# Kernel tuning notes

Measured on AMD Instinct MI355X. Metric: run time of the kernel, lower is better.

## Reference

```python
import jax, jax.numpy as jnp
import numpy as np

DIM = 256
HEADS = 8
DIM_HEAD = 32
INNER = HEADS * DIM_HEAD  # 256
EPS = 1e-5


def layer_norm(x, g, b):
    mu = jnp.mean(x, axis=-1, keepdims=True)
    var = jnp.var(x, axis=-1, keepdims=True)
    return (x - mu) * jax.lax.rsqrt(var + EPS) * g + b


def setup_inputs() -> dict:
    key = jax.random.key(0)
    ks = jax.random.split(key, 8)
    b, l, gx, gy, w1, w2 = 2, 5, 6, 8, 8, 8
    B, N = b * gx * gy, l * w1 * w2  # 96, 320
    x = jax.random.normal(ks[0], (b, l, gx, gy, w1, w2, DIM), dtype=jnp.float32)
    # context is the additive attention bias: [B, N, heads*N] -> (B,h,N,N)
    context = jax.random.normal(ks[1], (B, N, HEADS * N), dtype=jnp.float32) * 0.1
    s = 1.0 / np.sqrt(DIM)
    w_q = jax.random.normal(ks[2], (DIM, INNER), dtype=jnp.float32) * s
    w_kv = jax.random.normal(ks[3], (DIM, 2 * INNER), dtype=jnp.float32) * s
    w_out = jax.random.normal(ks[4], (INNER, DIM_HEAD), dtype=jnp.float32) * (1.0 / np.sqrt(INNER))
    ln_g = jnp.ones((DIM,), dtype=jnp.float32)
    ln_b = jnp.zeros((DIM,), dtype=jnp.float32)
    return {"x": x, "context": context, "w_q": w_q, "w_kv": w_kv,
            "w_out": w_out, "ln_g": ln_g, "ln_b": ln_b}


def reference(x, context, w_q, w_kv, w_out, ln_g, ln_b):
    b, l, gx, gy, w1, w2, d = x.shape
    # 'b l x y w1 w2 d -> (b x y) (l w1 w2) d'
    xs = jnp.transpose(x, (0, 2, 3, 1, 4, 5, 6)).reshape(b * gx * gy, l * w1 * w2, d)
    B, N, D = xs.shape
    xs = layer_norm(xs, ln_g, ln_b)
    q = (xs @ w_q).reshape(B, N, HEADS, DIM_HEAD).transpose(0, 2, 1, 3)   # b h n d
    kv = xs @ w_kv
    k, v = jnp.split(kv, 2, axis=-1)
    k = k.reshape(B, N, HEADS, DIM_HEAD).transpose(0, 2, 1, 3)
    v = v.reshape(B, N, HEADS, DIM_HEAD).transpose(0, 2, 1, 3)
    # bias mode with context: dots = q k^T (unscaled, faithful to source) + bias
    dots = jnp.einsum('bhnd,bhmd->bhnm', q, k)
    bias = context.reshape(B, N, HEADS, N).transpose(0, 2, 1, 3)          # b h n m
    dots = dots + bias
    attn = jax.nn.softmax(dots, axis=-1)
    out = jnp.einsum('bhnm,bhmd->bhnd', attn, v)                          # b h n d
    # 'b h (l w1 w2) d -> b l w1 w2 (h d)'
    out = out.transpose(0, 2, 1, 3).reshape(B, l, w1, w2, INNER)
    out = out @ w_out                                                     # -> dim_head
    # '(b x y) l w1 w2 d -> b l x y w1 w2 d'
    out = out.reshape(b, gx, gy, l, w1, w2, DIM_HEAD).transpose(0, 3, 1, 2, 4, 5, 6)
    return out
```

## Files before the change

### kernel.cpp

```cpp
#include <hip/hip_runtime.h>
#include <hip/hip_bf16.h>

#define BWIN 96
#define NTOK 320
#define DIMX 256
#define HEADS 8
#define DH 32
#define INNER 256
#define CTXW 2560
#define MPAD 328
#define ROWS_T 30720

typedef __bf16 bf16x8 __attribute__((ext_vector_type(8)));
typedef __bf16 bf16x4 __attribute__((ext_vector_type(4)));
typedef float f32x4 __attribute__((ext_vector_type(4)));

__global__ __launch_bounds__(256) void k_pre(
    const float* __restrict__ wq, const float* __restrict__ wkv,
    const float* __restrict__ x, const float* __restrict__ g,
    const float* __restrict__ bt, __bf16* __restrict__ wT,
    __bf16* __restrict__ y)
{
    const int t = threadIdx.x;
    if (blockIdx.x < 768) {
        const int col = blockIdx.x;
        float v;
        if (col < 256)      v = wq[t * 256 + col];
        else if (col < 512) v = wkv[t * 512 + (col - 256)];
        else                v = wkv[t * 512 + 256 + (col - 512)];
        wT[(size_t)col * 256 + t] = (__bf16)v;
        return;
    }
    const int wave = t >> 6, lane = t & 63;
    const int row = (blockIdx.x - 768) * 4 + wave;
    const int bb = row / NTOK, n = row % NTOK;
    const int b_idx = bb / 48, x_idx = (bb % 48) >> 3, y_idx = bb & 7;
    const int l_idx = n >> 6, w1_idx = (n >> 3) & 7, w2_idx = n & 7;
    const size_t src =
        ((((((size_t)b_idx * 5 + l_idx) * 6 + x_idx) * 8 + y_idx) * 8 + w1_idx) * 8 + w2_idx) * (size_t)DIMX;

    const float4 xv = *(const float4*)(x + src + lane * 4);
    float s = xv.x + xv.y + xv.z + xv.w;
    float ss = xv.x * xv.x + xv.y * xv.y + xv.z * xv.z + xv.w * xv.w;
    #pragma unroll
    for (int o = 32; o > 0; o >>= 1) {
        s += __shfl_xor(s, o);
        ss += __shfl_xor(ss, o);
    }
    const float mu = s * (1.0f / DIMX);
    const float var = ss * (1.0f / DIMX) - mu * mu;
    const float rsig = rsqrtf(var + 1e-5f);
    const float4 g4 = *(const float4*)(g + lane * 4);
    const float4 b4 = *(const float4*)(bt + lane * 4);
    bf16x4 yo;
    yo[0] = (__bf16)((xv.x - mu) * rsig * g4.x + b4.x);
    yo[1] = (__bf16)((xv.y - mu) * rsig * g4.y + b4.y);
    yo[2] = (__bf16)((xv.z - mu) * rsig * g4.z + b4.z);
    yo[3] = (__bf16)((xv.w - mu) * rsig * g4.w + b4.w);
    *(bf16x4*)(y + (size_t)row * DIMX + lane * 4) = yo;
}

__global__ __launch_bounds__(256) void k_qkv(
    const __bf16* __restrict__ y, const __bf16* __restrict__ wT,
    __bf16* __restrict__ qhb, __bf16* __restrict__ khb, __bf16* __restrict__ vhb)
{
    __shared__ __bf16 yls[128][40];
    __shared__ __bf16 wls[128][40];
    const int t = threadIdx.x, wave = t >> 6, lane = t & 63;
    const int lr = lane & 15, lg = lane >> 4;
    const int wm = wave & 1, wn = wave >> 1;
    const int rbase = blockIdx.x * 128;
    const int cbase = blockIdx.y * 128;

    f32x4 acc[4][4];
    #pragma unroll
    for (int im = 0; im < 4; ++im)
        #pragma unroll
        for (int jn = 0; jn < 4; ++jn) acc[im][jn] = (f32x4){0.f, 0.f, 0.f, 0.f};

    const int srow = t >> 1, sseg = (t & 1) * 16;
    #pragma unroll
    for (int ks = 0; ks < 8; ++ks) {
        __syncthreads();
        #pragma unroll
        for (int j = 0; j < 2; ++j) {
            *(bf16x8*)&yls[srow][sseg + j * 8] =
                *(const bf16x8*)(y + (size_t)(rbase + srow) * DIMX + ks * 32 + sseg + j * 8);
            *(bf16x8*)&wls[srow][sseg + j * 8] =
                *(const bf16x8*)(wT + (size_t)(cbase + srow) * DIMX + ks * 32 + sseg + j * 8);
        }
        __syncthreads();

        bf16x8 yfr[4], wfr[4];
        #pragma unroll
        for (int jn = 0; jn < 4; ++jn) yfr[jn] = *(const bf16x8*)&yls[wm * 64 + jn * 16 + lr][lg * 8];
        #pragma unroll
        for (int im = 0; im < 4; ++im) wfr[im] = *(const bf16x8*)&wls[wn * 64 + im * 16 + lr][lg * 8];
        #pragma unroll
        for (int im = 0; im < 4; ++im)
            #pragma unroll
            for (int jn = 0; jn < 4; ++jn)
                acc[im][jn] = __builtin_amdgcn_mfma_f32_16x16x32_bf16(wfr[im], yfr[jn], acc[im][jn], 0, 0, 0);
    }

    #pragma unroll
    for (int im = 0; im < 4; ++im) {
        const int g = cbase + wn * 64 + im * 16 + lg * 4;
        const int which = g >> 8;
        __bf16* buf = (which == 0) ? qhb : (which == 1) ? khb : vhb;
        const int hh = (g & 255) >> 5, d = g & 31;
        #pragma unroll
        for (int jn = 0; jn < 4; ++jn) {
            const int row = rbase + wm * 64 + jn * 16 + lr;
            const int bb2 = row / NTOK, n2 = row % NTOK;
            bf16x4 p;
            #pragma unroll
            for (int i = 0; i < 4; ++i) p[i] = (__bf16)acc[im][jn][i];
            *(bf16x4*)(buf + ((size_t)(bb2 * 8 + hh) * NTOK + n2) * DH + d) = p;
        }
    }
}

__global__ __launch_bounds__(256) void k_vw(
    const __bf16* __restrict__ vhb, const float* __restrict__ wout,
    __bf16* __restrict__ vwt)
{
    const int t = threadIdx.x, wave = t >> 6, lane = t & 63;
    const int lr = lane & 15, lg = lane >> 4;
    const int bb = blockIdx.x, h = blockIdx.y;
    const int m0 = wave * 80;

    bf16x8 afr[2];
    #pragma unroll
    for (int rt = 0; rt < 2; ++rt)
        #pragma unroll
        for (int j = 0; j < 8; ++j)
            afr[rt][j] = (__bf16)wout[(h * 32 + lg * 8 + j) * 32 + rt * 16 + lr];

    const __bf16* vbase = vhb + (size_t)(bb * 8 + h) * NTOK * DH + lg * 8;
    __bf16* obase = vwt + ((size_t)(bb * HEADS + h) * DH) * NTOK;

    #pragma unroll
    for (int mt = 0; mt < 5; ++mt) {
        const int m = m0 + mt * 16 + lr;
        const bf16x8 bfr = *(const bf16x8*)(vbase + (size_t)m * DH);
        #pragma unroll
        for (int rt = 0; rt < 2; ++rt) {
            const f32x4 d4 = __builtin_amdgcn_mfma_f32_16x16x32_bf16(
                afr[rt], bfr, (f32x4){0.f, 0.f, 0.f, 0.f}, 0, 0, 0);
            #pragma unroll
            for (int i = 0; i < 4; ++i) {
                const int drow = rt * 16 + lg * 4 + i;
                obase[(size_t)drow * NTOK + m0 + mt * 16 + lr] = (__bf16)d4[i];
            }
        }
    }
}

__global__ __launch_bounds__(128) void k_attn(
    const __bf16* __restrict__ qhb, const __bf16* __restrict__ khb,
    const __bf16* __restrict__ vwt, const float* __restrict__ ctx,
    float* __restrict__ part)
{
    __shared__ __bf16 kls[NTOK][DH];
    __shared__ __bf16 vwls[DH][MPAD];
    __shared__ __bf16 ctxls[2][16][MPAD];
    const int t = threadIdx.x, wave = t >> 6, lane = t & 63;
    const int lr = lane & 15, lg = lane >> 4;
    const int h = blockIdx.x & 7, bb = blockIdx.x >> 3;
    const size_t panel = (size_t)(bb * 8 + h);

    const __bf16* kpan = khb + panel * NTOK * DH;
    #pragma unroll
    for (int i = 0; i < 10; ++i) {
        const int idx = i * 128 + t;
        *(bf16x8*)&kls[idx >> 2][(idx & 3) * 8] = *(const bf16x8*)(kpan + idx * 8);
    }
    const __bf16* vpan = vwt + panel * DH * NTOK;
    #pragma unroll
    for (int i = 0; i < 10; ++i) {
        const int idx = i * 128 + t;
        const int r = idx / 40, c = (idx % 40) * 8;
        *(bf16x8*)&vwls[r][c] = *(const bf16x8*)(vpan + r * NTOK + c);
    }
    __syncthreads();

    const float* cpan = ctx + (size_t)bb * NTOK * CTXW + h * NTOK;
    const __bf16* qpan = qhb + panel * NTOK * DH;
    float* ppan = part + ((size_t)h * ROWS_T + (size_t)bb * NTOK) * DH;

    float4 creg[20];
    {
        const float* cb = cpan + (size_t)(wave * 16) * CTXW;
        #pragma unroll
        for (int j = 0; j < 20; ++j) {
            const int f = j * 64 + lane, r = f / 80, c = f % 80;
            creg[j] = *(const float4*)(cb + (size_t)r * CTXW + c * 4);
        }
    }

    for (int it = 0; it < 10; ++it) {
        const int nw = (it * 2 + wave) * 16;

        #pragma unroll
        for (int j = 0; j < 20; ++j) {
            const int f = j * 64 + lane, r = f / 80, c = f % 80;
            bf16x4 b;
            b[0] = (__bf16)creg[j].x; b[1] = (__bf16)creg[j].y;
            b[2] = (__bf16)creg[j].z; b[3] = (__bf16)creg[j].w;
            *(bf16x4*)&ctxls[wave][r][c * 4] = b;
        }
        if (it < 9) {
            const float* cb = cpan + (size_t)((it * 2 + 2 + wave) * 16) * CTXW;
            #pragma unroll
            for (int j = 0; j < 20; ++j) {
                const int f = j * 64 + lane, r = f / 80, c = f % 80;
                creg[j] = *(const float4*)(cb + (size_t)r * CTXW + c * 4);
            }
        }

        const bf16x8 qfrag = *(const bf16x8*)(qpan + (size_t)(nw + lr) * DH + lg * 8);

        f32x4 s[20];
        #pragma unroll
        for (int mt = 0; mt < 20; ++mt) {
            const bf16x8 kfrag = *(const bf16x8*)&kls[mt * 16 + lr][lg * 8];
            s[mt] = __builtin_amdgcn_mfma_f32_16x16x32_bf16(kfrag, qfrag,
                                                            (f32x4){0.f, 0.f, 0.f, 0.f}, 0, 0, 0);
        }

        #pragma unroll
        for (int mt = 0; mt < 20; ++mt) {
            const bf16x4 c4 = *(const bf16x4*)&ctxls[wave][lr][mt * 16 + lg * 4];
            #pragma unroll
            for (int i = 0; i < 4; ++i) s[mt][i] += (float)c4[i];
        }

        float mx = -3e38f;
        #pragma unroll
        for (int mt = 0; mt < 20; ++mt)
            #pragma unroll
            for (int i = 0; i < 4; ++i) mx = fmaxf(mx, s[mt][i]);
        mx = fmaxf(mx, __shfl_xor(mx, 16));
        mx = fmaxf(mx, __shfl_xor(mx, 32));

        float sum = 0.f;
        #pragma unroll
        for (int mt = 0; mt < 20; ++mt) {
            bf16x4 p4;
            #pragma unroll
            for (int i = 0; i < 4; ++i) {
                const float e = __expf(s[mt][i] - mx);
                sum += e;
                p4[i] = (__bf16)e;
            }
            *(bf16x4*)&ctxls[wave][lr][mt * 16 + lg * 4] = p4;
        }
        sum += __shfl_xor(sum, 16);
        sum += __shfl_xor(sum, 32);
        const float rinv = 1.0f / sum;

        f32x4 o0 = {0.f, 0.f, 0.f, 0.f}, o1 = {0.f, 0.f, 0.f, 0.f};
        #pragma unroll
        for (int ks = 0; ks < 10; ++ks) {
            const bf16x8 pfrag = *(const bf16x8*)&ctxls[wave][lr][ks * 32 + lg * 8];
            const bf16x8 vf0 = *(const bf16x8*)&vwls[lr][ks * 32 + lg * 8];
            const bf16x8 vf1 = *(const bf16x8*)&vwls[16 + lr][ks * 32 + lg * 8];
            o0 = __builtin_amdgcn_mfma_f32_16x16x32_bf16(vf0, pfrag, o0, 0, 0, 0);
            o1 = __builtin_amdgcn_mfma_f32_16x16x32_bf16(vf1, pfrag, o1, 0, 0, 0);
        }

        float* pdst = ppan + (size_t)(nw + lr) * DH + lg * 4;
        f32x4 r0, r1;
        #pragma unroll
        for (int i = 0; i < 4; ++i) { r0[i] = o0[i] * rinv; r1[i] = o1[i] * rinv; }
        *(f32x4*)(pdst)      = r0;
        *(f32x4*)(pdst + 16) = r1;
    }
}

__global__ __launch_bounds__(256) void k_red(
    const float* __restrict__ part, float* __restrict__ out)
{
    const int idx = blockIdx.x * 256 + threadIdx.x;
    const int row = idx >> 3, q4 = (idx & 7) * 4;
    f32x4 a = {0.f, 0.f, 0.f, 0.f};
    #pragma unroll
    for (int h = 0; h < HEADS; ++h) {
        const f32x4 p = *(const f32x4*)(part + ((size_t)h * ROWS_T + row) * DH + q4);
        #pragma unroll
        for (int i = 0; i < 4; ++i) a[i] += p[i];
    }
    const int bb = row / NTOK, n = row % NTOK;
    const int b_idx = bb / 48, x_idx = (bb % 48) >> 3, y_idx = bb & 7;
    const int l_idx = n >> 6, w1_idx = (n >> 3) & 7, w2_idx = n & 7;
    const size_t dst =
        ((((((size_t)b_idx * 5 + l_idx) * 6 + x_idx) * 8 + y_idx) * 8 + w1_idx) * 8 + w2_idx) * (size_t)DH;
    *(f32x4*)(out + dst + q4) = a;
}

extern "C" void kernel_launch(void* const* d_in, const int* in_sizes, int n_in,
                              void* d_out, int out_size, void* d_ws, size_t ws_size,
                              hipStream_t stream) {
    const float* x    = (const float*)d_in[0];
    const float* ctx  = (const float*)d_in[1];
    const float* wq   = (const float*)d_in[2];
    const float* wkv  = (const float*)d_in[3];
    const float* wout = (const float*)d_in[4];
    const float* ln_g = (const float*)d_in[5];
    const float* ln_b = (const float*)d_in[6];
    float* out = (float*)d_out;

    const size_t SEG = (size_t)BWIN * NTOK * INNER;
    __bf16* qhb = (__bf16*)d_ws;
    __bf16* khb = qhb + SEG;
    __bf16* vhb = khb + SEG;
    __bf16* yb  = vhb + SEG;
    __bf16* wT  = yb + SEG;
    __bf16* vwt = wT + 768 * 256;
    float*  part = (float*)(vwt + SEG);

    const int ROWS = BWIN * NTOK;
    k_pre<<<768 + ROWS / 4, 256, 0, stream>>>(wq, wkv, x, ln_g, ln_b, wT, yb);
    k_qkv<<<dim3(ROWS / 128, 6), 256, 0, stream>>>(yb, wT, qhb, khb, vhb);
    k_vw<<<dim3(BWIN, HEADS), 256, 0, stream>>>(vhb, wout, vwt);
    k_attn<<<BWIN * HEADS, 128, 0, stream>>>(qhb, khb, vwt, ctx, part);
    k_red<<<ROWS * 8 / 256, 256, 0, stream>>>(part, out);
}
```

Measured before the change: 162.8 us.

## Fuse V·Wout projection into attention kernel and read K fragments from global

Removes the separate k_vw launch: each attention block now computes its V·Wout panel directly into shared memory with MFMA, avoiding the vwt workspace round trip. The K panel is no longer staged in LDS; kfrag loads come straight from global memory (likely cached in L1/L2). This saves one kernel launch and a global write/read of the projected V and frees LDS, possibly improving occupancy. The cost is redundant global K loads in every iteration and extra MFMA work at the start of each attention block.

```diff
diff --git a/kernel.cpp b/kernel.cpp
--- a/kernel.cpp
+++ b/kernel.cpp
@@ -121,48 +121,11 @@
     }
 }
 
-__global__ __launch_bounds__(256) void k_vw(
-    const __bf16* __restrict__ vhb, const float* __restrict__ wout,
-    __bf16* __restrict__ vwt)
-{
-    const int t = threadIdx.x, wave = t >> 6, lane = t & 63;
-    const int lr = lane & 15, lg = lane >> 4;
-    const int bb = blockIdx.x, h = blockIdx.y;
-    const int m0 = wave * 80;
-
-    bf16x8 afr[2];
-    #pragma unroll
-    for (int rt = 0; rt < 2; ++rt)
-        #pragma unroll
-        for (int j = 0; j < 8; ++j)
-            afr[rt][j] = (__bf16)wout[(h * 32 + lg * 8 + j) * 32 + rt * 16 + lr];
-
-    const __bf16* vbase = vhb + (size_t)(bb * 8 + h) * NTOK * DH + lg * 8;
-    __bf16* obase = vwt + ((size_t)(bb * HEADS + h) * DH) * NTOK;
-
-    #pragma unroll
-    for (int mt = 0; mt < 5; ++mt) {
-        const int m = m0 + mt * 16 + lr;
-        const bf16x8 bfr = *(const bf16x8*)(vbase + (size_t)m * DH);
-        #pragma unroll
-        for (int rt = 0; rt < 2; ++rt) {
-            const f32x4 d4 = __builtin_amdgcn_mfma_f32_16x16x32_bf16(
-                afr[rt], bfr, (f32x4){0.f, 0.f, 0.f, 0.f}, 0, 0, 0);
-            #pragma unroll
-            for (int i = 0; i < 4; ++i) {
-                const int drow = rt * 16 + lg * 4 + i;
-                obase[(size_t)drow * NTOK + m0 + mt * 16 + lr] = (__bf16)d4[i];
-            }
-        }
-    }
-}
-
 __global__ __launch_bounds__(128) void k_attn(
     const __bf16* __restrict__ qhb, const __bf16* __restrict__ khb,
-    const __bf16* __restrict__ vwt, const float* __restrict__ ctx,
-    float* __restrict__ part)
+    const __bf16* __restrict__ vhb, const float* __restrict__ wout,
+    const float* __restrict__ ctx, float* __restrict__ part)
 {
-    __shared__ __bf16 kls[NTOK][DH];
     __shared__ __bf16 vwls[DH][MPAD];
     __shared__ __bf16 ctxls[2][16][MPAD];
     const int t = threadIdx.x, wave = t >> 6, lane = t & 63;
@@ -170,23 +133,33 @@
     const int h = blockIdx.x & 7, bb = blockIdx.x >> 3;
     const size_t panel = (size_t)(bb * 8 + h);
 
-    const __bf16* kpan = khb + panel * NTOK * DH;
-    #pragma unroll
-    for (int i = 0; i < 10; ++i) {
-        const int idx = i * 128 + t;
-        *(bf16x8*)&kls[idx >> 2][(idx & 3) * 8] = *(const bf16x8*)(kpan + idx * 8);
-    }
-    const __bf16* vpan = vwt + panel * DH * NTOK;
-    #pragma unroll
-    for (int i = 0; i < 10; ++i) {
-        const int idx = i * 128 + t;
-        const int r = idx / 40, c = (idx % 40) * 8;
-        *(bf16x8*)&vwls[r][c] = *(const bf16x8*)(vpan + r * NTOK + c);
+    {
+        bf16x8 afr[2];
+        #pragma unroll
+        for (int rt = 0; rt < 2; ++rt)
+            #pragma unroll
+            for (int j = 0; j < 8; ++j)
+                afr[rt][j] = (__bf16)wout[(h * 32 + lg * 8 + j) * 32 + rt * 16 + lr];
+        const __bf16* vbase = vhb + panel * NTOK * DH + lg * 8;
+        #pragma unroll
+        for (int mt = 0; mt < 10; ++mt) {
+            const int m = wave * 160 + mt * 16 + lr;
+            const bf16x8 bfr = *(const bf16x8*)(vbase + (size_t)m * DH);
+            #pragma unroll
+            for (int rt = 0; rt < 2; ++rt) {
+                const f32x4 d4 = __builtin_amdgcn_mfma_f32_16x16x32_bf16(
+                    afr[rt], bfr, (f32x4){0.f, 0.f, 0.f, 0.f}, 0, 0, 0);
+                #pragma unroll
+                for (int i = 0; i < 4; ++i)
+                    vwls[rt * 16 + lg * 4 + i][wave * 160 + mt * 16 + lr] = (__bf16)d4[i];
+            }
+        }
     }
     __syncthreads();
 
     const float* cpan = ctx + (size_t)bb * NTOK * CTXW + h * NTOK;
     const __bf16* qpan = qhb + panel * NTOK * DH;
+    const __bf16* kpan = khb + panel * NTOK * DH;
     float* ppan = part + ((size_t)h * ROWS_T + (size_t)bb * NTOK) * DH;
 
     float4 creg[20];
@@ -224,7 +197,7 @@
         f32x4 s[20];
         #pragma unroll
         for (int mt = 0; mt < 20; ++mt) {
-            const bf16x8 kfrag = *(const bf16x8*)&kls[mt * 16 + lr][lg * 8];
+            const bf16x8 kfrag = *(const bf16x8*)(kpan + (size_t)(mt * 16 + lr) * DH + lg * 8);
             s[mt] = __builtin_amdgcn_mfma_f32_16x16x32_bf16(kfrag, qfrag,
                                                             (f32x4){0.f, 0.f, 0.f, 0.f}, 0, 0, 0);
         }
@@ -317,13 +290,11 @@
     __bf16* vhb = khb + SEG;
     __bf16* yb  = vhb + SEG;
     __bf16* wT  = yb + SEG;
-    __bf16* vwt = wT + 768 * 256;
-    float*  part = (float*)(vwt + SEG);
+    float*  part = (float*)(wT + 768 * 256);
 
     const int ROWS = BWIN * NTOK;
     k_pre<<<768 + ROWS / 4, 256, 0, stream>>>(wq, wkv, x, ln_g, ln_b, wT, yb);
     k_qkv<<<dim3(ROWS / 128, 6), 256, 0, stream>>>(yb, wT, qhb, khb, vhb);
-    k_vw<<<dim3(BWIN, HEADS), 256, 0, stream>>>(vhb, wout, vwt);
-    k_attn<<<BWIN * HEADS, 128, 0, stream>>>(qhb, khb, vwt, ctx, part);
+    k_attn<<<BWIN * HEADS, 128, 0, stream>>>(qhb, khb, vhb, wout, ctx, part);
     k_red<<<ROWS * 8 / 256, 256, 0, stream>>>(part, out);
 }
```

New measurement: 154.6 us. -5.1%, faster.
